# Kernel tuning notes

Hardware: AMD Instinct MI355X
Metric: run time of the kernel (lower is better)

## Reference

```python
import jax, jax.numpy as jnp
import numpy as np

B, T, D_IN, H1, H2 = 32, 2048, 1024, 512, 32


def setup_inputs() -> dict:
    key = jax.random.key(0)
    ks = jax.random.split(key, 8)
    avf_out = jax.random.normal(ks[0], (B, T, D_IN), dtype=jnp.float32)
    # seq_len in [1, T] so every sample has a non-empty slice (matches torch usage)
    seq_len = jax.random.randint(ks[1], (B,), 1, T + 1, dtype=jnp.int32)
    s = 0.02
    W1 = jax.random.normal(ks[2], (D_IN, H1), dtype=jnp.float32) * s
    b1 = jnp.zeros((H1,), dtype=jnp.float32)
    W2 = jax.random.normal(ks[3], (H1, H2), dtype=jnp.float32) * s
    b2 = jnp.zeros((H2,), dtype=jnp.float32)
    W3 = jax.random.normal(ks[4], (H2, 1), dtype=jnp.float32) * s
    b3 = jnp.zeros((1,), dtype=jnp.float32)
    return {"avf_out": avf_out, "W1": W1, "b1": b1, "W2": W2, "b2": b2,
            "W3": W3, "b3": b3, "seq_len": seq_len}


def reference(avf_out, W1, b1, W2, b2, W3, b3, seq_len):
    h = jax.nn.relu(jnp.einsum('btd,dh->bth', avf_out, W1) + b1)
    h = jnp.einsum('bth,hk->btk', h, W2) + b2
    logits = jax.nn.sigmoid(jnp.einsum('btk,ko->bto', h, W3) + b3)[..., 0]  # [B, T]
    # ragged per-sample top-k (k = seq_len//16 + 1 over first seq_len entries) + mean,
    # vectorized via masked descending sort + cumsum (no per-sample loop)
    Tn = logits.shape[1]
    valid = jnp.arange(Tn)[None, :] < seq_len[:, None]            # [B, T]
    NEG = jnp.float32(-1.0)  # below sigmoid range, so padded slots never enter top-k
    masked = jnp.where(valid, logits, NEG)
    sorted_desc = -jnp.sort(-masked, axis=1)                      # [B, T] descending
    csum = jnp.cumsum(sorted_desc, axis=1)
    k = seq_len // 16 + 1                                         # k <= seq_len always
    topk_sum = jnp.take_along_axis(csum, (k - 1)[:, None].astype(jnp.int32), axis=1)[:, 0]
    return topk_sum / k.astype(logits.dtype)                      # [B]
```

## Files before the change

### kernel.cpp

```cpp
#include <hip/hip_runtime.h>

typedef __bf16 bf16;
typedef __bf16 bf16x4 __attribute__((ext_vector_type(4)));
typedef __bf16 bf16x8 __attribute__((ext_vector_type(8)));
typedef float f32x4 __attribute__((ext_vector_type(4)));

#define K_TOT 1024
#define N_TOT 512
#define T_SEQ 2048
#define NB 32
#define M_TILE 160
#define MAX_J 13
#define NBLK_TGT 256

__device__ __forceinline__ void async16(const void* g, void* l) {
    __builtin_amdgcn_global_load_lds(
        (const __attribute__((address_space(1))) unsigned int*)g,
        (__attribute__((address_space(3))) unsigned int*)l, 16, 0, 0);
}

__global__ __launch_bounds__(256) void transpose_prep(
        const float* __restrict__ W1, bf16* __restrict__ W1T,
        const float* __restrict__ W2, const float* __restrict__ b2,
        const float* __restrict__ W3, const float* __restrict__ b3,
        const int* __restrict__ seq_len,
        float* __restrict__ v, int* __restrict__ tiles, int* __restrict__ done) {
    __shared__ float tile[32][33];
    __shared__ int nb2[32], off2[32], Ls[32];
    const int t = threadIdx.x;
    const int k0 = blockIdx.x * 32;
    const int n0 = blockIdx.y * 32;
#pragma unroll
    for (int p = 0; p < 4; p++) {
        int kl = p * 8 + (t >> 5);
        int nl = t & 31;
        tile[kl][nl] = W1[(k0 + kl) * 512 + n0 + nl];
    }
    __syncthreads();
#pragma unroll
    for (int p = 0; p < 4; p++) {
        int nl = p * 8 + (t >> 5);
        int kl = t & 31;
        W1T[(n0 + nl) * 1024 + k0 + kl] = (bf16)tile[kl][nl];
    }

    if (blockIdx.x == 0 && blockIdx.y == 0) {
        for (int h = t; h < 512; h += 256) {
            float s = 0.f;
#pragma unroll
            for (int c = 0; c < 32; c++) s += W2[h * 32 + c] * W3[c];
            v[h] = s;
        }
        if (t == 0) {
            float cc = b3[0];
            for (int c = 0; c < 32; c++) cc += b2[c] * W3[c];
            v[512] = cc;
        }
        if (t < 32) {
            int L = seq_len[t];
            Ls[t] = L;
            nb2[t] = (L + M_TILE - 1) / M_TILE;
            done[t] = 0;
        }
        __syncthreads();
        if (t == 0) {
            int tot = 0;
            for (int i = 0; i < 32; i++) tot += nb2[i];
            while (tot < NBLK_TGT) {
                int best = -1, bestr = 1;
                for (int i = 0; i < 32; i++) {
                    int r = (Ls[i] + nb2[i] - 1) / nb2[i];
                    if (r > bestr && nb2[i] < Ls[i]) { bestr = r; best = i; }
                }
                if (best < 0) break;
                nb2[best]++; tot++;
            }
            int a = 0;
            for (int i = 0; i < 32; i++) { off2[i] = a; a += nb2[i]; }
            tiles[0] = a;
        }
        __syncthreads();
        for (int idx = t; idx < 32 * 256; idx += 256) {
            int b = idx >> 8, j = idx & 255;
            int nb = nb2[b];
            if (j < nb) {
                int L = Ls[b];
                int q = L / nb, r = L % nb;
                int start = j * q + (j < r ? j : r);
                int nrows = q + (j < r ? 1 : 0);
                tiles[1 + off2[b] + j] = (b << 19) | (start << 8) | nrows;
            }
        }
    }
}

__device__ __forceinline__ int sw_idx(int row, int e) {
    return row * 64 + (((e >> 3) ^ (row & 7)) << 3) + (e & 7);
}

__global__ __launch_bounds__(512, 2) void gemm_fused(const float* __restrict__ A,
                                                     const bf16* __restrict__ W1T,
                                                     const float* __restrict__ b1,
                                                     const float* __restrict__ v,
                                                     const int* __restrict__ tiles,
                                                     const int* __restrict__ seq_len,
                                                     int* __restrict__ done,
                                                     float* __restrict__ logits,
                                                     float* __restrict__ out) {
    __shared__ bf16 smem[M_TILE * 64 + 2 * N_TOT * 64];
    bf16* As = smem;
    bf16* Bs0 = smem + M_TILE * 64;
    bf16* Bs1 = Bs0 + N_TOT * 64;

    const int nact = tiles[0];
    if ((int)blockIdx.x >= nact) return;
    const int w = tiles[1 + blockIdx.x];
    const int bsmp = w >> 19;
    const int start = (w >> 8) & 0x7FF;
    const int mrows = w & 0xFF;
    const int m0 = bsmp * T_SEQ + start;

    const int t = threadIdx.x;
    const int wave = t >> 6, lane = t & 63;
    const int q = lane >> 4, l15 = lane & 15;
    const int wm = wave >> 2, wn = wave & 3;

    const int c16 = t & 15, r0 = t >> 4;
    const float* agp[5];
#pragma unroll
    for (int p = 0; p < 5; p++)
        agp[p] = A + (size_t)(m0 + r0 + p * 32) * K_TOT + c16 * 4;

    const int bl_row = wave * 64 + (lane >> 3);
    const int bl_chunk = (lane & 7) ^ ((lane >> 3) & 7);
    const bf16* bgp = W1T + (size_t)bl_row * K_TOT + bl_chunk * 8;

    f32x4 acc[5][8] = {};
    float4 av[5];

    auto loadA = [&](int k0) {
#pragma unroll
        for (int p = 0; p < 5; p++)
            if (r0 + p * 32 < mrows) av[p] = *(const float4*)(agp[p] + k0);
    };
    auto asyncB = [&](int k0, bf16* bs) {
#pragma unroll
        for (int j = 0; j < 8; j++)
            async16(bgp + k0 + (size_t)j * 8 * K_TOT, bs + (wave * 64 + j * 8) * 64);
    };
    auto writeA = [&]() {
#pragma unroll
        for (int p = 0; p < 5; p++) {
            if (r0 + p * 32 >= mrows) continue;
            bf16x4 wv;
            wv[0] = (bf16)av[p].x; wv[1] = (bf16)av[p].y;
            wv[2] = (bf16)av[p].z; wv[3] = (bf16)av[p].w;
            int row = r0 + p * 32;
            int chunk = c16 >> 1;
            int idx = row * 64 + ((chunk ^ (row & 7)) << 3) + (c16 & 1) * 4;
            *(bf16x4*)(&As[idx]) = wv;
        }
    };
    auto mfma_phase = [&](const bf16* bs) {
#pragma unroll
        for (int kk = 0; kk < 64; kk += 32) {
            const int e = kk + q * 8;
            bf16x8 af[5];
#pragma unroll
            for (int mi = 0; mi < 5; mi++)
                af[mi] = *(const bf16x8*)(&As[sw_idx(wm * 80 + mi * 16 + l15, e)]);
#pragma unroll
            for (int nh = 0; nh < 8; nh += 4) {
                bf16x8 bfv[4];
#pragma unroll
                for (int ni = 0; ni < 4; ni++)
                    bfv[ni] = *(const bf16x8*)(&bs[sw_idx(wn * 128 + (nh + ni) * 16 + l15, e)]);
#pragma unroll
                for (int mi = 0; mi < 5; mi++)
#pragma unroll
                    for (int ni = 0; ni < 4; ni++)
                        acc[mi][nh + ni] = __builtin_amdgcn_mfma_f32_16x16x32_bf16(
                            af[mi], bfv[ni], acc[mi][nh + ni], 0, 0, 0);
            }
        }
    };

    loadA(0);
    asyncB(0, Bs0);
    writeA();
    __syncthreads();

#pragma unroll 1
    for (int k = 0; k < 16; k++) {
        bf16* bcur = (k & 1) ? Bs1 : Bs0;
        bf16* bnxt = (k & 1) ? Bs0 : Bs1;
        if (k < 15) {
            loadA((k + 1) * 64);
            asyncB((k + 1) * 64, bnxt);
        }
        mfma_phase(bcur);
        __syncthreads();
        if (k < 15) {
            writeA();
            __syncthreads();
        }
    }

    float bb[8], vv[8];
#pragma unroll
    for (int ni = 0; ni < 8; ni++) {
        int col = wn * 128 + ni * 16 + l15;
        bb[ni] = b1[col];
        vv[ni] = v[col];
    }
    const float cconst = v[512];

    float* part = (float*)smem;

#pragma unroll
    for (int mi = 0; mi < 5; mi++) {
#pragma unroll
        for (int r = 0; r < 4; r++) {
            float s = 0.f;
#pragma unroll
            for (int ni = 0; ni < 8; ni++)
                s += fmaxf(acc[mi][ni][r] + bb[ni], 0.f) * vv[ni];
            s += __shfl_xor(s, 1);
            s += __shfl_xor(s, 2);
            s += __shfl_xor(s, 4);
            s += __shfl_xor(s, 8);
            if (l15 == 0) {
                int row = wm * 80 + mi * 16 + q * 4 + r;
                part[row * 4 + wn] = s;
            }
        }
    }
    __syncthreads();
    if (t < mrows) {
        float s = part[t * 4] + part[t * 4 + 1] + part[t * 4 + 2] + part[t * 4 + 3] + cconst;
        logits[m0 + t] = 1.f / (1.f + __expf(-s));
    }

    const int L = seq_len[bsmp];

    float* vals  = (float*)smem;
    int*   redi  = (int*)(vals + 2048);
    unsigned* mnx = (unsigned*)(redi + 16);
    float* redf  = (float*)(mnx + 16);
    int*   wflag = (int*)(redf + 8);

    __syncthreads();
    if (t == 0) {
        __threadfence();
        int old = atomicAdd(&done[bsmp], mrows);
        int win = (old + mrows == L);
        if (win) __threadfence();
        *wflag = win;
    }
    __syncthreads();
    if (!*wflag) return;

    const int kk = (L >> 4) + 1;
    const float* p = logits + bsmp * T_SEQ;

    unsigned mn = 0x3f800000u, mx = 0u;
    for (int i = t; i < L; i += 512) {
        float x = p[i];
        vals[i] = x;
        unsigned u = __float_as_uint(x);
        mn = min(mn, u); mx = max(mx, u);
    }
#pragma unroll
    for (int m = 32; m >= 1; m >>= 1) {
        mn = min(mn, (unsigned)__shfl_xor((int)mn, m));
        mx = max(mx, (unsigned)__shfl_xor((int)mx, m));
    }
    if (lane == 0) { mnx[wave] = mn; mnx[8 + wave] = mx; }
    __syncthreads();
    unsigned lo = mnx[0], hi = mnx[8];
#pragma unroll
    for (int w8 = 1; w8 < 8; w8++) {
        lo = min(lo, mnx[w8]); hi = max(hi, mnx[8 + w8]);
    }
    __syncthreads();

    int rb = 0;
    while (lo < hi) {
        unsigned wd = hi - lo;
        unsigned t1 = wd / 3u + 1u;
        unsigned m1 = lo + t1;
        unsigned m2 = lo + (wd - wd / 3u);
        if (m2 < m1) m2 = m1;
        float f1 = __uint_as_float(m1), f2 = __uint_as_float(m2);
        int c1 = 0, c2 = 0;
        for (int i = t; i < L; i += 512) {
            float x = vals[i];
            c1 += (x >= f1) ? 1 : 0;
            c2 += (x >= f2) ? 1 : 0;
        }
        int packed = (c1 << 12) | c2;
#pragma unroll
        for (int m = 32; m >= 1; m >>= 1) packed += __shfl_xor(packed, m);
        if (lane == 0) redi[(rb & 1) * 8 + wave] = packed;
        __syncthreads();
        int tot = 0;
#pragma unroll
        for (int w8 = 0; w8 < 8; w8++) tot += redi[(rb & 1) * 8 + w8];
        int C2 = tot & 0xFFF, C1 = tot >> 12;
        if (C2 >= kk)      { lo = m2; }
        else if (C1 >= kk) { lo = m1; hi = m2 - 1; }
        else               { hi = m1 - 1; }
        rb++;
    }
    const float thr = __uint_as_float(lo);

    int cg = 0; float sg = 0.f;
    for (int i = t; i < L; i += 512) {
        float x = vals[i];
        if (x > thr) { cg += 1; sg += x; }
    }
#pragma unroll
    for (int m = 32; m >= 1; m >>= 1) {
        cg += __shfl_xor(cg, m);
        sg += __shfl_xor(sg, m);
    }
    if (lane == 0) { redi[(rb & 1) * 8 + wave] = cg; redf[wave] = sg; }
    __syncthreads();
    if (t == 0) {
        int cgt = 0; float sgt = 0.f;
#pragma unroll
        for (int w8 = 0; w8 < 8; w8++) { cgt += redi[(rb & 1) * 8 + w8]; sgt += redf[w8]; }
        out[bsmp] = (sgt + (float)(kk - cgt) * thr) / (float)kk;
    }
}

extern "C" void kernel_launch(void* const* d_in, const int* in_sizes, int n_in,
                              void* d_out, int out_size, void* d_ws, size_t ws_size,
                              hipStream_t stream) {
    const float* avf = (const float*)d_in[0];
    const float* W1  = (const float*)d_in[1];
    const float* b1  = (const float*)d_in[2];
    const float* W2  = (const float*)d_in[3];
    const float* b2  = (const float*)d_in[4];
    const float* W3  = (const float*)d_in[5];
    const float* b3  = (const float*)d_in[6];
    const int* seq_len = (const int*)d_in[7];
    float* out = (float*)d_out;

    char* ws = (char*)d_ws;
    bf16*  W1T    = (bf16*)ws;
    float* v      = (float*)(ws + (1 << 20));
    int*   tiles  = (int*)(ws + (1 << 20) + 4096);
    int*   done   = (int*)(ws + (1 << 20) + 8192);
    float* logits = (float*)(ws + (1 << 20) + 12288);

    transpose_prep<<<dim3(32, 16), 256, 0, stream>>>(W1, W1T, W2, b2, W3, b3,
                                                     seq_len, v, tiles, done);
    gemm_fused<<<NB * MAX_J, 512, 0, stream>>>(avf, W1T, b1, v, tiles, seq_len,
                                               done, logits, out);
}
```

Measured before the change: 460.7 us.

## Balance tile rows with uniform cap and skip MFMAs on empty row groups

Replaces the serial greedy tile-splitting loop with a parallel search for the smallest uniform rows-per-tile cap that keeps the total tile count within the block target. Each block then gets fewer, more even rows. The GEMM kernel also precomputes per-row liveness and skips LDS A-fragment loads and MFMA issue for 16-row groups that lie beyond the tile's valid rows. This avoids wasted matrix work on partial tiles, at the cost of wave-uniform branches inside the hot loop.

New measurement: 394.7 us. 14.3% less time.

```diff
diff --git a/kernel.cpp b/kernel.cpp
--- a/kernel.cpp
+++ b/kernel.cpp
@@ -26,7 +26,6 @@
         const int* __restrict__ seq_len,
         float* __restrict__ v, int* __restrict__ tiles, int* __restrict__ done) {
     __shared__ float tile[32][33];
-    __shared__ int nb2[32], off2[32], Ls[32];
     const int t = threadIdx.x;
     const int k0 = blockIdx.x * 32;
     const int n0 = blockIdx.y * 32;
@@ -45,6 +44,7 @@
     }
 
     if (blockIdx.x == 0 && blockIdx.y == 0) {
+        __shared__ int Ls[32], nb2[32], off2[32], rbest;
         for (int h = t; h < 512; h += 256) {
             float s = 0.f;
 #pragma unroll
@@ -55,26 +55,24 @@
             float cc = b3[0];
             for (int c = 0; c < 32; c++) cc += b2[c] * W3[c];
             v[512] = cc;
+            rbest = M_TILE;
         }
         if (t < 32) {
-            int L = seq_len[t];
-            Ls[t] = L;
-            nb2[t] = (L + M_TILE - 1) / M_TILE;
+            Ls[t] = seq_len[t];
             done[t] = 0;
         }
         __syncthreads();
+        if (t < M_TILE) {
+            int R = t + 1, S = 0;
+#pragma unroll 4
+            for (int i = 0; i < 32; i++) S += (Ls[i] + R - 1) / R;
+            if (S <= NBLK_TGT) atomicMin(&rbest, R);
+        }
+        __syncthreads();
+        const int R = rbest;
+        if (t < 32) nb2[t] = (Ls[t] + R - 1) / R;
+        __syncthreads();
         if (t == 0) {
-            int tot = 0;
-            for (int i = 0; i < 32; i++) tot += nb2[i];
-            while (tot < NBLK_TGT) {
-                int best = -1, bestr = 1;
-                for (int i = 0; i < 32; i++) {
-                    int r = (Ls[i] + nb2[i] - 1) / nb2[i];
-                    if (r > bestr && nb2[i] < Ls[i]) { bestr = r; best = i; }
-                }
-                if (best < 0) break;
-                nb2[best]++; tot++;
-            }
             int a = 0;
             for (int i = 0; i < 32; i++) { off2[i] = a; a += nb2[i]; }
             tiles[0] = a;
@@ -126,10 +124,16 @@
     const int wm = wave >> 2, wn = wave & 3;
 
     const int c16 = t & 15, r0 = t >> 4;
+    bool alive[5];
     const float* agp[5];
 #pragma unroll
-    for (int p = 0; p < 5; p++)
+    for (int p = 0; p < 5; p++) {
+        alive[p] = (r0 + p * 32) < mrows;
         agp[p] = A + (size_t)(m0 + r0 + p * 32) * K_TOT + c16 * 4;
+    }
+    bool mlive[5];
+#pragma unroll
+    for (int p = 0; p < 5; p++) mlive[p] = (wm * 80 + p * 16) < mrows;
 
     const int bl_row = wave * 64 + (lane >> 3);
     const int bl_chunk = (lane & 7) ^ ((lane >> 3) & 7);
@@ -141,7 +145,7 @@
     auto loadA = [&](int k0) {
 #pragma unroll
         for (int p = 0; p < 5; p++)
-            if (r0 + p * 32 < mrows) av[p] = *(const float4*)(agp[p] + k0);
+            if (alive[p]) av[p] = *(const float4*)(agp[p] + k0);
     };
     auto asyncB = [&](int k0, bf16* bs) {
 #pragma unroll
@@ -151,7 +155,7 @@
     auto writeA = [&]() {
 #pragma unroll
         for (int p = 0; p < 5; p++) {
-            if (r0 + p * 32 >= mrows) continue;
+            if (!alive[p]) continue;
             bf16x4 wv;
             wv[0] = (bf16)av[p].x; wv[1] = (bf16)av[p].y;
             wv[2] = (bf16)av[p].z; wv[3] = (bf16)av[p].w;
@@ -168,7 +172,8 @@
             bf16x8 af[5];
 #pragma unroll
             for (int mi = 0; mi < 5; mi++)
-                af[mi] = *(const bf16x8*)(&As[sw_idx(wm * 80 + mi * 16 + l15, e)]);
+                if (mlive[mi])
+                    af[mi] = *(const bf16x8*)(&As[sw_idx(wm * 80 + mi * 16 + l15, e)]);
 #pragma unroll
             for (int nh = 0; nh < 8; nh += 4) {
                 bf16x8 bfv[4];
@@ -177,10 +182,11 @@
                     bfv[ni] = *(const bf16x8*)(&bs[sw_idx(wn * 128 + (nh + ni) * 16 + l15, e)]);
 #pragma unroll
                 for (int mi = 0; mi < 5; mi++)
-#pragma unroll
-                    for (int ni = 0; ni < 4; ni++)
-                        acc[mi][nh + ni] = __builtin_amdgcn_mfma_f32_16x16x32_bf16(
-                            af[mi], bfv[ni], acc[mi][nh + ni], 0, 0, 0);
+                    if (mlive[mi])
+#pragma unroll
+                        for (int ni = 0; ni < 4; ni++)
+                            acc[mi][nh + ni] = __builtin_amdgcn_mfma_f32_16x16x32_bf16(
+                                af[mi], bfv[ni], acc[mi][nh + ni], 0, 0, 0);
             }
         }
     };
```
